# Kernel optimization log

Measured on AMD Instinct MI355X. Metric: run time of the kernel, lower is better.

Reference implementation:

```python
import jax, jax.numpy as jnp
import numpy as np

N_QUBITS = 10
Q_DEPTH = 6
MAX_LAYERS = 15
DIM = 2 ** N_QUBITS


def _apply_1q(s, U, w):
    # s: (B, 2^n) real statevector (circuit uses only H/RY/CNOT, all real).
    # Wire 0 is the most-significant bit (PennyLane convention).
    a, b = 2 ** w, 2 ** (N_QUBITS - 1 - w)
    s = s.reshape(-1, a, 2, b)
    if U.ndim == 2:  # gate shared across batch
        s = jnp.einsum('ij,Bajb->Baib', U, s)
    else:            # per-sample gate, U: (B,2,2)
        s = jnp.einsum('Bij,Bajb->Baib', U, s)
    return s.reshape(-1, DIM)


def _apply_cnot(s, c, t):
    # CNOT, control c < target t
    s = s.reshape(-1, 2 ** c, 2, 2 ** (t - c - 1), 2, 2 ** (N_QUBITS - 1 - t))
    s = jnp.stack([s[:, :, 0], jnp.flip(s[:, :, 1], axis=3)], axis=2)
    return s.reshape(-1, DIM)


def _ry(theta):
    # RY(theta) = [[cos t/2, -sin t/2], [sin t/2, cos t/2]]; theta scalar or (B,)
    c, si = jnp.cos(theta / 2.0), jnp.sin(theta / 2.0)
    return jnp.stack([jnp.stack([c, -si], -1), jnp.stack([si, c], -1)], -2)


def _quantum_net(q_in, q_params):
    # q_in: (B, n_qubits) rotation angles; q_params: (max_layers*n_qubits,)
    B = q_in.shape[0]
    qw = q_params.reshape(MAX_LAYERS, N_QUBITS)
    s = jnp.zeros((B, DIM), q_in.dtype).at[:, 0].set(1.0)  # |0...0>
    H = jnp.array([[1.0, 1.0], [1.0, -1.0]], q_in.dtype) / jnp.sqrt(jnp.asarray(2.0, q_in.dtype))
    for w in range(N_QUBITS):
        s = _apply_1q(s, H, w)
    for w in range(N_QUBITS):
        s = _apply_1q(s, _ry(q_in[:, w]), w)
    for k in range(Q_DEPTH):
        for i in range(0, N_QUBITS - 1, 2):
            s = _apply_cnot(s, i, i + 1)
        for i in range(1, N_QUBITS - 1, 2):
            s = _apply_cnot(s, i, i + 1)
        for w in range(N_QUBITS):
            s = _apply_1q(s, _ry(qw[k + 1, w]), w)
    probs = s * s
    # <Z_w> = P(bit_w = 0) - P(bit_w = 1)
    z = []
    for w in range(N_QUBITS):
        p = probs.reshape(-1, 2 ** w, 2, 2 ** (N_QUBITS - 1 - w)).sum(axis=(1, 3))
        z.append(p[:, 0] - p[:, 1])
    return jnp.stack(z, axis=1)  # (B, n_qubits)


def setup_inputs() -> dict:
    key = jax.random.key(0)
    ks = jax.random.split(key, 6)
    B, F, NQ, NC = 8192, 512, N_QUBITS, 2
    q_delta = 0.01
    return {
        'input_features': jax.random.normal(ks[0], (B, F), jnp.float32),
        'W_pre': jax.random.normal(ks[1], (NQ, F), jnp.float32) / np.sqrt(F),
        'b_pre': jnp.zeros((NQ,), jnp.float32),
        'q_params': q_delta * jax.random.normal(ks[2], (MAX_LAYERS * NQ,), jnp.float32),
        'W_post': jax.random.normal(ks[3], (NC, NQ), jnp.float32) / np.sqrt(NQ),
        'b_post': jnp.zeros((NC,), jnp.float32),
    }


def reference(input_features, W_pre, b_pre, q_params, W_post, b_post):
    pre_out = input_features @ W_pre.T + b_pre          # (B, n_qubits)
    q_in = jnp.tanh(pre_out) * (np.pi / 2.0)            # scale to [-pi/2, pi/2]
    q_out = _quantum_net(q_in, q_params)                # (B, n_qubits) PauliZ expvals
    return q_out @ W_post.T + b_post                    # (B, n_classes)
```

## Files before the change

kernel.cpp:

```cpp
#include <hip/hip_runtime.h>
#include <math.h>


#define NQ   10
#define NREG 16
#define DIM  1024

typedef _Float16 f16;
typedef _Float16 f16x8 __attribute__((ext_vector_type(8)));
typedef float    f32x4 __attribute__((ext_vector_type(4)));

template<int BB>
__device__ __forceinline__ void ry_lane(float (&s)[NREG], int lane, float c, float si) {
    float sgn = ((lane >> BB) & 1) ? si : -si;
    #pragma unroll
    for (int r = 0; r < NREG; ++r) {
        float o = __shfl_xor(s[r], 1 << BB);
        s[r] = fmaf(sgn, o, c * s[r]);
    }
}
template<int P>
__device__ __forceinline__ void ry_reg(float (&s)[NREG], float c, float si) {
    const int m = 1 << P;
    #pragma unroll
    for (int r = 0; r < NREG; ++r) {
        if ((r & m) == 0) {
            float a = s[r], b = s[r + m];
            s[r]     = fmaf(c, a, -si * b);
            s[r + m] = fmaf(si, a,  c * b);
        }
    }
}
__device__ __forceinline__ void cnot_5_6(float (&s)[NREG], int lane) {
    bool sel = (lane & 1) != 0;
    #pragma unroll
    for (int r = 0; r < 8; ++r) {
        float a = s[r], b = s[r + 8];
        s[r]     = sel ? b : a;
        s[r + 8] = sel ? a : b;
    }
}
template<int PC, int PT>
__device__ __forceinline__ void cnot_reg(float (&s)[NREG]) {
    #pragma unroll
    for (int r = 0; r < NREG; ++r) {
        if (((r >> PC) & 1) && !((r >> PT) & 1)) {
            float t = s[r];
            s[r] = s[r ^ (1 << PT)];
            s[r ^ (1 << PT)] = t;
        }
    }
}
__device__ __forceinline__ void perm_even(float (&s)[NREG], int lane) {
    int src = lane ^ (((((lane >> 5) & 1) << 4)) | ((((lane >> 3) & 1) << 2)) | (((lane >> 1) & 1)));
    #pragma unroll
    for (int r = 0; r < NREG; ++r) s[r] = __shfl(s[r], src);
}
__device__ __forceinline__ void perm_odd(float (&s)[NREG], int lane) {
    int src = lane ^ (((((lane >> 4) & 1) << 3)) | ((((lane >> 2) & 1) << 1)));
    #pragma unroll
    for (int r = 0; r < NREG; ++r) s[r] = __shfl(s[r], src);
}

#define APPLY_RY_ALL(CARR, SARR, BASE)                                        \
    { float c_, s_;                                                           \
      c_=__shfl(CARR,(BASE)+0); s_=__shfl(SARR,(BASE)+0); ry_lane<5>(s,lane,c_,s_); \
      c_=__shfl(CARR,(BASE)+1); s_=__shfl(SARR,(BASE)+1); ry_lane<4>(s,lane,c_,s_); \
      c_=__shfl(CARR,(BASE)+2); s_=__shfl(SARR,(BASE)+2); ry_lane<3>(s,lane,c_,s_); \
      c_=__shfl(CARR,(BASE)+3); s_=__shfl(SARR,(BASE)+3); ry_lane<2>(s,lane,c_,s_); \
      c_=__shfl(CARR,(BASE)+4); s_=__shfl(SARR,(BASE)+4); ry_lane<1>(s,lane,c_,s_); \
      c_=__shfl(CARR,(BASE)+5); s_=__shfl(SARR,(BASE)+5); ry_lane<0>(s,lane,c_,s_); \
      c_=__shfl(CARR,(BASE)+6); s_=__shfl(SARR,(BASE)+6); ry_reg<3>(s,c_,s_);       \
      c_=__shfl(CARR,(BASE)+7); s_=__shfl(SARR,(BASE)+7); ry_reg<2>(s,c_,s_);       \
      c_=__shfl(CARR,(BASE)+8); s_=__shfl(SARR,(BASE)+8); ry_reg<1>(s,c_,s_);       \
      c_=__shfl(CARR,(BASE)+9); s_=__shfl(SARR,(BASE)+9); ry_reg<0>(s,c_,s_); }

__device__ __forceinline__ void async16(const void* g, void* l) {
    __builtin_amdgcn_global_load_lds(
        (const __attribute__((address_space(1))) void*)g,
        (__attribute__((address_space(3))) void*)l, 16, 0, 0);
}

#define BARRIER() do { __builtin_amdgcn_s_barrier(); __builtin_amdgcn_sched_barrier(0); } while (0)
#define VMCNT8()  asm volatile("s_waitcnt vmcnt(8)" ::: "memory")
#define VMCNT0()  asm volatile("s_waitcnt vmcnt(0)" ::: "memory")

__global__ __launch_bounds__(256) void ka_prepare(
    const float* __restrict__ X, const float* __restrict__ Wpre,
    const float* __restrict__ bpre, const float* __restrict__ qp,
    f16* __restrict__ psi0, f16* __restrict__ Arm, float* __restrict__ z, int B)
{
    const int tid = threadIdx.x, lane = tid & 63, wv = tid >> 6;

    {
        int idx = blockIdx.x * 256 + tid;
        if (idx < 8192 * NQ) z[idx] = 0.0f;
    }

    {
        int sample = blockIdx.x * 4 + wv;
        if (sample < B) {
            const float* xrow = X + (size_t)sample * 512;
            float4 x0 = ((const float4*)xrow)[lane];
            float4 x1 = ((const float4*)xrow)[64 + lane];
            float acc[NQ];
            #pragma unroll
            for (int q = 0; q < NQ; ++q) {
                const float* wr = Wpre + q * 512;
                float4 w0 = ((const float4*)wr)[lane];
                float4 w1 = ((const float4*)wr)[64 + lane];
                float a = x0.x * w0.x;
                a = fmaf(x0.y, w0.y, a); a = fmaf(x0.z, w0.z, a); a = fmaf(x0.w, w0.w, a);
                a = fmaf(x1.x, w1.x, a); a = fmaf(x1.y, w1.y, a);
                a = fmaf(x1.z, w1.z, a); a = fmaf(x1.w, w1.w, a);
                acc[q] = a;
            }
            #pragma unroll
            for (int q = 0; q < NQ; ++q) {
                float v = acc[q];
                #pragma unroll
                for (int d = 32; d >= 1; d >>= 1) v += __shfl_xor(v, d);
                acc[q] = v;
            }
            float pre = acc[0];
            #pragma unroll
            for (int q = 1; q < NQ; ++q) pre = (lane == q) ? acc[q] : pre;
            float c45 = 0.0f, s45 = 0.0f;
            if (lane < NQ) {
                float th = tanhf(pre + bpre[lane]) * 1.5707963267948966f;
                sincosf(0.5f * th + 0.7853981633974483f, &s45, &c45);
            }
            float lv = 1.0f;
            #pragma unroll
            for (int w = 0; w < 6; ++w) {
                float f0 = __shfl(c45, w), f1 = __shfl(s45, w);
                lv *= ((lane >> (5 - w)) & 1) ? f1 : f0;
            }
            float c6 = __shfl(c45, 6), s6 = __shfl(s45, 6);
            float c7 = __shfl(c45, 7), s7 = __shfl(s45, 7);
            float c8 = __shfl(c45, 8), s8 = __shfl(s45, 8);
            float c9 = __shfl(c45, 9), s9 = __shfl(s45, 9);
            float g01[4] = {c6 * c7, c6 * s7, s6 * c7, s6 * s7};
            float g23[4] = {c8 * c9, c8 * s9, s8 * c9, s8 * s9};
            union { f16 h[16]; float4 v[2]; } u;
            #pragma unroll
            for (int r = 0; r < NREG; ++r)
                u.h[r] = (f16)(lv * g01[r >> 2] * g23[r & 3]);
            float4* dst = (float4*)((char*)psi0 + (size_t)sample * 2048 + lane * 32);
            dst[0] = u.v[0];
            dst[1] = u.v[1];
        }
    }

    if (wv < 2) {
        int row = blockIdx.x * 2 + wv;
        if (row < DIM) {
            float cw = 1.0f, swn = 0.0f;
            if (lane < 60) {
                float s_, c_;
                sincosf(0.5f * qp[10 + lane], &s_, &c_);
                cw = c_; swn = -s_;
            }
            float s[NREG];
            int srcLane = row >> 4, srcReg = row & 15;
            #pragma unroll
            for (int r = 0; r < NREG; ++r)
                s[r] = (lane == srcLane && r == srcReg) ? 1.0f : 0.0f;
            for (int kk = 6; kk >= 1; --kk) {
                APPLY_RY_ALL(cw, swn, (kk - 1) * 10);
                perm_odd(s, lane);
                cnot_5_6(s, lane);
                cnot_reg<2, 1>(s);
                perm_even(s, lane);
                cnot_reg<3, 2>(s);
                cnot_reg<1, 0>(s);
            }
            union { f16 h[16]; float4 v[2]; } u;
            #pragma unroll
            for (int r = 0; r < NREG; ++r) u.h[r] = (f16)s[r];
            float4* dst = (float4*)((char*)Arm + (size_t)row * 2048 + lane * 32);
            dst[0] = u.v[0];
            dst[1] = u.v[1];
        }
    }
}

__global__ __launch_bounds__(256) void kb_gemm_measure(
    const f16* __restrict__ psi0, const f16* __restrict__ Arm,
    float* __restrict__ z)
{
    __shared__ __align__(16) char smem[65536];
    const int tid = threadIdx.x, lane = tid & 63, wv = tid >> 6;
    const int mB = blockIdx.x & 63, nB = blockIdx.x >> 6;
    const size_t tM = (size_t)mB * 128, tN = (size_t)nB * 128;
    f16* As0 = (f16*)smem;
    f16* Bs0 = (f16*)(smem + 16384);
    f16* As1 = (f16*)(smem + 32768);
    f16* Bs1 = (f16*)(smem + 49152);
    const int wm = (wv >> 1) * 64, wn = (wv & 1) * 64;

    f32x4 acc[4][4] = {};

    const f16* ga[4]; const f16* gb[4]; int ldso[4];
    #pragma unroll
    for (int p = 0; p < 4; ++p) {
        int slot = p * 256 + tid;
        int row = slot >> 3, gp = slot & 7, g = gp ^ (row & 7);
        ga[p] = psi0 + (tM + row) * 1024 + g * 8;
        gb[p] = Arm  + (tN + row) * 1024 + g * 8;
        ldso[p] = slot * 16;
    }

    auto stage = [&](f16* Ab, f16* Bb, int kt) {
        #pragma unroll
        for (int p = 0; p < 4; ++p) async16(ga[p] + kt, (char*)Ab + ldso[p]);
        #pragma unroll
        for (int p = 0; p < 4; ++p) async16(gb[p] + kt, (char*)Bb + ldso[p]);
    };
    auto compute = [&](const f16* Ab, const f16* Bb) {
        #pragma unroll
        for (int ks = 0; ks < 2; ++ks) {
            f16x8 af[4], bf[4];
            const int gpb = ks * 4 + (lane >> 4);
            const int gpx = gpb ^ (lane & 7);
            #pragma unroll
            for (int i = 0; i < 4; ++i) {
                int rowA = wm + i * 16 + (lane & 15);
                af[i] = *(const f16x8*)(Ab + rowA * 64 + gpx * 8);
            }
            #pragma unroll
            for (int j = 0; j < 4; ++j) {
                int rowB = wn + j * 16 + (lane & 15);
                bf[j] = *(const f16x8*)(Bb + rowB * 64 + gpx * 8);
            }
            #pragma unroll
            for (int i = 0; i < 4; ++i)
                #pragma unroll
                for (int j = 0; j < 4; ++j)
                    acc[i][j] = __builtin_amdgcn_mfma_f32_16x16x32_f16(af[i], bf[j], acc[i][j], 0, 0, 0);
        }
    };

    stage(As0, Bs0, 0);
    #pragma unroll 1
    for (int kt = 0; kt < 896; kt += 128) {
        stage(As1, Bs1, kt + 64);
        VMCNT8();
        BARRIER();
        compute(As0, Bs0);
        BARRIER();
        stage(As0, Bs0, kt + 128);
        VMCNT8();
        BARRIER();
        compute(As1, Bs1);
        BARRIER();
    }
    stage(As1, Bs1, 960);
    VMCNT8();
    BARRIER();
    compute(As0, Bs0);
    VMCNT0();
    BARRIER();
    compute(As1, Bs1);

    __syncthreads();
    float* zbuf = (float*)smem;
    float* zb = zbuf + (wn ? 1280 : 0);
    const float sg0 = (nB & 4) ? -1.0f : 1.0f;
    const float sg1 = (nB & 2) ? -1.0f : 1.0f;
    const float sg2 = (nB & 1) ? -1.0f : 1.0f;
    const float sg3 = wn ? -1.0f : 1.0f;

    #pragma unroll
    for (int i = 0; i < 4; ++i) {
        #pragma unroll
        for (int t = 0; t < 4; ++t) {
            float p0 = acc[i][0][t] * acc[i][0][t];
            float p1 = acc[i][1][t] * acc[i][1][t];
            float p2 = acc[i][2][t] * acc[i][2][t];
            float p3 = acc[i][3][t] * acc[i][3][t];
            float t0  = (p0 + p1) + (p2 + p3);
            float tw5 = (p0 - p1) + (p2 - p3);
            float tw4 = (p0 + p1) - (p2 + p3);
            float s1 = __shfl_xor(t0, 1);
            float Av = t0 + s1;
            float Bv = (lane & 1) ? s1 - t0 : t0 - s1;
            float sA = __shfl_xor(Av, 2), sB = __shfl_xor(Bv, 2);
            float AP = Av + sA;
            float AM = (lane & 2) ? sA - Av : Av - sA;
            float BP = Bv + sB;
            float sAP = __shfl_xor(AP, 4), sAM = __shfl_xor(AM, 4), sBP = __shfl_xor(BP, 4);
            float APP = AP + sAP;
            float APM = (lane & 4) ? sAP - AP : AP - sAP;
            float AMP = AM + sAM;
            float BPP = BP + sBP;
            float a1 = __shfl_xor(APP, 8), a2 = __shfl_xor(APM, 8);
            float a3 = __shfl_xor(AMP, 8), a4 = __shfl_xor(BPP, 8);
            float T0 = APP + a1;
            float S6 = (lane & 8) ? a1 - APP : APP - a1;
            float S7 = APM + a2;
            float S8 = AMP + a3;
            float S9 = BPP + a4;
            float T5 = tw5, T4 = tw4;
            T5 += __shfl_xor(T5, 1); T5 += __shfl_xor(T5, 2);
            T5 += __shfl_xor(T5, 4); T5 += __shfl_xor(T5, 8);
            T4 += __shfl_xor(T4, 1); T4 += __shfl_xor(T4, 2);
            T4 += __shfl_xor(T4, 4); T4 += __shfl_xor(T4, 8);
            if ((lane & 15) == 0) {
                int row = wm + i * 16 + (lane >> 4) * 4 + t;
                float* d = zb + row * 10;
                d[0] = sg0 * T0; d[1] = sg1 * T0; d[2] = sg2 * T0; d[3] = sg3 * T0;
                d[4] = T4; d[5] = T5;
                d[6] = S6; d[7] = S7; d[8] = S8; d[9] = S9;
            }
        }
    }
    __syncthreads();
    for (int idx = tid; idx < 1280; idx += 256) {
        float v = zbuf[idx] + zbuf[1280 + idx];
        int row = idx / 10, w = idx - row * 10;
        atomicAdd(&z[((size_t)tM + row) * 10 + w], v);
    }
}

__global__ __launch_bounds__(256) void kc_post(
    const float* __restrict__ z, const float* __restrict__ Wpost,
    const float* __restrict__ bpost, float* __restrict__ out, int B)
{
    int gid = blockIdx.x * 256 + threadIdx.x;
    if (gid >= B) return;
    const float* zp = z + (size_t)gid * NQ;
    float o0 = bpost[0], o1 = bpost[1];
    #pragma unroll
    for (int w = 0; w < NQ; ++w) {
        float zw = zp[w];
        o0 = fmaf(zw, Wpost[w], o0);
        o1 = fmaf(zw, Wpost[NQ + w], o1);
    }
    out[(size_t)gid * 2 + 0] = o0;
    out[(size_t)gid * 2 + 1] = o1;
}

template<int BC, int BT>
__device__ __forceinline__ void cnot_lane(float (&s)[NREG], int lane) {
    int src = ((lane >> BC) & 1) ? (lane ^ (1 << BT)) : lane;
    #pragma unroll
    for (int r = 0; r < NREG; ++r) s[r] = __shfl(s[r], src);
}

__global__ __launch_bounds__(256) void hybrid_head_fallback(
    const float* __restrict__ X, const float* __restrict__ Wpre,
    const float* __restrict__ bpre, const float* __restrict__ qp,
    const float* __restrict__ Wpost, const float* __restrict__ bpost,
    float* __restrict__ out, int B)
{
    const int lane = threadIdx.x & 63;
    const int wave = threadIdx.x >> 6;
    const int sample = blockIdx.x * 4 + wave;
    if (sample >= B) return;

    const float* xrow = X + (size_t)sample * 512;
    float4 x0 = ((const float4*)xrow)[lane];
    float4 x1 = ((const float4*)xrow)[64 + lane];
    float acc[NQ];
    #pragma unroll
    for (int q = 0; q < NQ; ++q) {
        const float* wr = Wpre + q * 512;
        float4 w0 = ((const float4*)wr)[lane];
        float4 w1 = ((const float4*)wr)[64 + lane];
        float a = x0.x * w0.x;
        a = fmaf(x0.y, w0.y, a); a = fmaf(x0.z, w0.z, a); a = fmaf(x0.w, w0.w, a);
        a = fmaf(x1.x, w1.x, a); a = fmaf(x1.y, w1.y, a);
        a = fmaf(x1.z, w1.z, a); a = fmaf(x1.w, w1.w, a);
        acc[q] = a;
    }
    #pragma unroll
    for (int q = 0; q < NQ; ++q) {
        float v = acc[q];
        #pragma unroll
        for (int d = 32; d >= 1; d >>= 1) v += __shfl_xor(v, d);
        acc[q] = v;
    }
    float pre = acc[0];
    #pragma unroll
    for (int q = 1; q < NQ; ++q) pre = (lane == q) ? acc[q] : pre;
    float cth = 1.0f, sth = 0.0f;
    if (lane < NQ) {
        float th = tanhf(pre + bpre[lane]) * 1.5707963267948966f;
        sincosf(0.5f * th, &sth, &cth);
    }
    float cw = 1.0f, sw = 0.0f;
    if (lane < 60) sincosf(0.5f * qp[10 + lane], &sw, &cw);

    float s[NREG];
    #pragma unroll
    for (int r = 0; r < NREG; ++r) s[r] = 0.03125f;
    APPLY_RY_ALL(cth, sth, 0);
    for (int k = 0; k < 6; ++k) {
        perm_even(s, lane);
        cnot_reg<3, 2>(s);
        cnot_reg<1, 0>(s);
        perm_odd(s, lane);
        cnot_5_6(s, lane);
        cnot_reg<2, 1>(s);
        APPLY_RY_ALL(cw, sw, k * 10);
    }
    float p[NREG], tot = 0.0f;
    #pragma unroll
    for (int r = 0; r < NREG; ++r) { p[r] = s[r] * s[r]; tot += p[r]; }
    float z[NQ];
    #pragma unroll
    for (int w = 0; w < 6; ++w) z[w] = ((lane >> (5 - w)) & 1) ? -tot : tot;
    z[6] = z[7] = z[8] = z[9] = 0.0f;
    #pragma unroll
    for (int r = 0; r < NREG; ++r) {
        z[6] += ((r >> 3) & 1) ? -p[r] : p[r];
        z[7] += ((r >> 2) & 1) ? -p[r] : p[r];
        z[8] += ((r >> 1) & 1) ? -p[r] : p[r];
        z[9] += ((r >> 0) & 1) ? -p[r] : p[r];
    }
    #pragma unroll
    for (int w = 0; w < NQ; ++w) {
        float v = z[w];
        #pragma unroll
        for (int d = 32; d >= 1; d >>= 1) v += __shfl_xor(v, d);
        z[w] = v;
    }
    if (lane < 2) {
        const float* wp = Wpost + lane * NQ;
        float o = bpost[lane];
        #pragma unroll
        for (int w = 0; w < NQ; ++w) o = fmaf(z[w], wp[w], o);
        out[(size_t)sample * 2 + lane] = o;
    }
}

extern "C" void kernel_launch(void* const* d_in, const int* in_sizes, int n_in,
                              void* d_out, int out_size, void* d_ws, size_t ws_size,
                              hipStream_t stream) {
    const float* X     = (const float*)d_in[0];
    const float* Wpre  = (const float*)d_in[1];
    const float* bpre  = (const float*)d_in[2];
    const float* qp    = (const float*)d_in[3];
    const float* Wpost = (const float*)d_in[4];
    const float* bpost = (const float*)d_in[5];
    float* out = (float*)d_out;
    int B = in_sizes[0] / 512;

    size_t psi0_b = (size_t)B * DIM * sizeof(f16);
    size_t arm_b  = (size_t)DIM * DIM * sizeof(f16);
    size_t z_b    = (size_t)B * NQ * sizeof(float);
    size_t need = psi0_b + arm_b + z_b;

    if (B != 8192 || ws_size < need) {
        hipLaunchKernelGGL(hybrid_head_fallback, dim3((B + 3) / 4), dim3(256), 0, stream,
                           X, Wpre, bpre, qp, Wpost, bpost, out, B);
        return;
    }

    char* ws = (char*)d_ws;
    f16*   psi0 = (f16*)ws;
    f16*   Arm  = (f16*)(ws + psi0_b);
    float* z    = (float*)(ws + psi0_b + arm_b);

    hipLaunchKernelGGL(ka_prepare, dim3(2048), dim3(256), 0, stream,
                       X, Wpre, bpre, qp, psi0, Arm, z, B);
    hipLaunchKernelGGL(kb_gemm_measure, dim3(512), dim3(256), 0, stream,
                       psi0, Arm, z);
    hipLaunchKernelGGL(kc_post, dim3(32), dim3(256), 0, stream,
                       z, Wpost, bpost, out, B);
}
```

Measured before the change: 118.4 us.

## Widen GEMM tile to 128x256 with 8 waves per block

```diff
diff --git a/kernel.cpp b/kernel.cpp
--- a/kernel.cpp
+++ b/kernel.cpp
@@ -82,7 +82,7 @@
 }
 
 #define BARRIER() do { __builtin_amdgcn_s_barrier(); __builtin_amdgcn_sched_barrier(0); } while (0)
-#define VMCNT8()  asm volatile("s_waitcnt vmcnt(8)" ::: "memory")
+#define VMCNT6()  asm volatile("s_waitcnt vmcnt(6)" ::: "memory")
 #define VMCNT0()  asm volatile("s_waitcnt vmcnt(0)" ::: "memory")
 
 __global__ __launch_bounds__(256) void ka_prepare(
@@ -185,37 +185,44 @@
     }
 }
 
-__global__ __launch_bounds__(256) void kb_gemm_measure(
+__global__ __launch_bounds__(512) void kb_gemm_measure(
     const f16* __restrict__ psi0, const f16* __restrict__ Arm,
     float* __restrict__ z)
 {
-    __shared__ __align__(16) char smem[65536];
+    __shared__ __align__(16) char smem[98304];
     const int tid = threadIdx.x, lane = tid & 63, wv = tid >> 6;
-    const int mB = blockIdx.x & 63, nB = blockIdx.x >> 6;
-    const size_t tM = (size_t)mB * 128, tN = (size_t)nB * 128;
+    const int mB = blockIdx.x >> 2, nB = blockIdx.x & 3;
+    const size_t tM = (size_t)mB * 128, tN = (size_t)nB * 256;
     f16* As0 = (f16*)smem;
     f16* Bs0 = (f16*)(smem + 16384);
-    f16* As1 = (f16*)(smem + 32768);
-    f16* Bs1 = (f16*)(smem + 49152);
-    const int wm = (wv >> 1) * 64, wn = (wv & 1) * 64;
+    f16* As1 = (f16*)(smem + 49152);
+    f16* Bs1 = (f16*)(smem + 65536);
+    const int wm = (wv >> 2) * 64, wn = (wv & 3) * 64;
 
     f32x4 acc[4][4] = {};
 
-    const f16* ga[4]; const f16* gb[4]; int ldso[4];
-    #pragma unroll
-    for (int p = 0; p < 4; ++p) {
-        int slot = p * 256 + tid;
+    const f16* ga[2]; int ldsoA[2];
+    const f16* gb[4]; int ldsoB[4];
+    #pragma unroll
+    for (int p = 0; p < 2; ++p) {
+        int slot = p * 512 + tid;
         int row = slot >> 3, gp = slot & 7, g = gp ^ (row & 7);
         ga[p] = psi0 + (tM + row) * 1024 + g * 8;
-        gb[p] = Arm  + (tN + row) * 1024 + g * 8;
-        ldso[p] = slot * 16;
+        ldsoA[p] = slot * 16;
+    }
+    #pragma unroll
+    for (int p = 0; p < 4; ++p) {
+        int slot = p * 512 + tid;
+        int row = slot >> 3, gp = slot & 7, g = gp ^ (row & 7);
+        gb[p] = Arm + (tN + row) * 1024 + g * 8;
+        ldsoB[p] = slot * 16;
     }
 
     auto stage = [&](f16* Ab, f16* Bb, int kt) {
         #pragma unroll
-        for (int p = 0; p < 4; ++p) async16(ga[p] + kt, (char*)Ab + ldso[p]);
-        #pragma unroll
-        for (int p = 0; p < 4; ++p) async16(gb[p] + kt, (char*)Bb + ldso[p]);
+        for (int p = 0; p < 2; ++p) async16(ga[p] + kt, (char*)Ab + ldsoA[p]);
+        #pragma unroll
+        for (int p = 0; p < 4; ++p) async16(gb[p] + kt, (char*)Bb + ldsoB[p]);
     };
     auto compute = [&](const f16* Ab, const f16* Bb) {
         #pragma unroll
@@ -245,18 +252,18 @@
     #pragma unroll 1
     for (int kt = 0; kt < 896; kt += 128) {
         stage(As1, Bs1, kt + 64);
-        VMCNT8();
+        VMCNT6();
         BARRIER();
         compute(As0, Bs0);
         BARRIER();
         stage(As0, Bs0, kt + 128);
-        VMCNT8();
+        VMCNT6();
         BARRIER();
         compute(As1, Bs1);
         BARRIER();
     }
     stage(As1, Bs1, 960);
-    VMCNT8();
+    VMCNT6();
     BARRIER();
     compute(As0, Bs0);
     VMCNT0();
@@ -265,11 +272,11 @@
 
     __syncthreads();
     float* zbuf = (float*)smem;
-    float* zb = zbuf + (wn ? 1280 : 0);
-    const float sg0 = (nB & 4) ? -1.0f : 1.0f;
-    const float sg1 = (nB & 2) ? -1.0f : 1.0f;
-    const float sg2 = (nB & 1) ? -1.0f : 1.0f;
-    const float sg3 = wn ? -1.0f : 1.0f;
+    float* zb = zbuf + (wv & 3) * 1280;
+    const float sg0 = (nB & 2)        ? -1.0f : 1.0f;
+    const float sg1 = (nB & 1)        ? -1.0f : 1.0f;
+    const float sg2 = ((wv >> 1) & 1) ? -1.0f : 1.0f;
+    const float sg3 = (wv & 1)        ? -1.0f : 1.0f;
 
     #pragma unroll
     for (int i = 0; i < 4; ++i) {
@@ -316,8 +323,8 @@
         }
     }
     __syncthreads();
-    for (int idx = tid; idx < 1280; idx += 256) {
-        float v = zbuf[idx] + zbuf[1280 + idx];
+    for (int idx = tid; idx < 1280; idx += 512) {
+        float v = (zbuf[idx] + zbuf[1280 + idx]) + (zbuf[2560 + idx] + zbuf[3840 + idx]);
         int row = idx / 10, w = idx - row * 10;
         atomicAdd(&z[((size_t)tM + row) * 10 + w], v);
     }
@@ -465,7 +472,7 @@
 
     hipLaunchKernelGGL(ka_prepare, dim3(2048), dim3(256), 0, stream,
                        X, Wpre, bpre, qp, psi0, Arm, z, B);
-    hipLaunchKernelGGL(kb_gemm_measure, dim3(512), dim3(256), 0, stream,
+    hipLaunchKernelGGL(kb_gemm_measure, dim3(256), dim3(512), 0, stream,
                        psi0, Arm, z);
     hipLaunchKernelGGL(kc_post, dim3(32), dim3(256), 0, stream,
                        z, Wpost, bpost, out, B);
```

New measurement: 117.6 us. Within noise of the previous version (-0.6%).
